# Kernel optimization log

Hardware: AMD Instinct MI355X
Metric: run time of the kernel (lower is better)

The kernel has to match this reference:

```python
import jax, jax.numpy as jnp
import numpy as np

NUM_BLOCKS = 32
B, S = 8, 2048


def setup_inputs() -> dict:
    key = jax.random.key(0)
    k1, k2, k3 = jax.random.split(key, 3)
    h = jax.random.uniform(k1, (B, S, NUM_BLOCKS, 4), dtype=jnp.float32)
    W = jax.random.uniform(k2, (B, S, NUM_BLOCKS, NUM_BLOCKS), dtype=jnp.float32)
    stim = jax.random.uniform(k3, (B, S, NUM_BLOCKS), dtype=jnp.float32)
    return {"h": h, "W": W, "stim": stim}


def _step(h, W, stim):
    nb = h.shape[-2]
    eye = jnp.eye(nb, dtype=W.dtype)
    W_no_self = W * (1.0 - eye)                      # zero self-connections
    # neighbor inflow: [b,s,i,j] @ [b,s,j,c] -> [b,s,i,c]
    inflow = jnp.einsum('bsij,bsjc->bsic', W_no_self, h)
    total_w = W_no_self.sum(axis=-1, keepdims=True) + 1e-8
    neigh = inflow / total_w                          # weighted neighbor mean

    E, P, G, L = h[..., 0], h[..., 1], h[..., 2], h[..., 3]
    En, Pn, Gn, Ln = neigh[..., 0], neigh[..., 1], neigh[..., 2], neigh[..., 3]

    clamp01 = lambda x: jnp.clip(x, 0.0, 1.0)
    E_new = clamp01(E + 0.3 * stim - 0.4 * P - 0.2 * G)
    P_new = clamp01(P + 0.5 * stim + 0.3 * (Pn - P) - 0.2 * E)
    G_new = clamp01(G + 0.4 * E * (1.0 - P) + 0.2 * (Gn - G) - 0.3 * P)
    good_neighbor = 0.5 * En + 0.5 * Gn
    L_new = clamp01(L + 0.4 * good_neighbor + 0.3 * (Ln - L) - 0.3 * P)

    h_new = jnp.stack([E_new, P_new, G_new, L_new], axis=-1)  # [b,s,nb,4]

    # pairwise euclidean distance over the 4 EPGL channels (torch.cdist p=2)
    diff = h_new[..., :, None, :] - h_new[..., None, :, :]    # [b,s,nb,nb,4]
    sq = jnp.sum(diff * diff, axis=-1)
    # safe sqrt: zero distance -> 0 (matches cdist; avoids nan grads)
    h_diff = jnp.where(sq > 0, jnp.sqrt(jnp.where(sq > 0, sq, 1.0)), 0.0)

    mutual_L = 0.5 * (L_new[..., :, None] + L_new[..., None, :])
    alpha, beta = 0.1 * mutual_L, 0.05
    W_new = W + alpha * h_diff - beta * W
    W_new = jnp.clip(W_new, 0.0, 1.0) * (1.0 - eye)
    return h_new, W_new


def reference(h, W, stim):
    return _step(h, W, stim)
```

## Files before the change

### kernel.cpp

```cpp
#include <hip/hip_runtime.h>

#define NB 32
#define WAVES_PER_BLOCK 4
#define TOKENS_PER_WAVE 4

__device__ __forceinline__ float clamp01(float x) {
    return fminf(fmaxf(x, 0.0f), 1.0f);
}

__device__ __forceinline__ void gload_lds16(const float* g, float* lds) {
    __builtin_amdgcn_global_load_lds(
        (const __attribute__((address_space(1))) void*)g,
        (__attribute__((address_space(3))) void*)lds, 16, 0, 0);
}
__device__ __forceinline__ void gload_lds4(const float* g, float* lds) {
    __builtin_amdgcn_global_load_lds(
        (const __attribute__((address_space(1))) void*)g,
        (__attribute__((address_space(3))) void*)lds, 4, 0, 0);
}

__device__ __forceinline__ void stage_token(
    const float* __restrict__ W, const float* __restrict__ h,
    int token, float* bufW, float* bufH, int lw)
{
    const float* Wt = W + (size_t)token * (NB * NB);
    #pragma unroll
    for (int k = 0; k < 4; ++k) {
        gload_lds16(Wt + (size_t)(k * 64 + lw) * 4, bufW + k * 256);
    }
    const float* ht = h + (size_t)token * (NB * 4);
    gload_lds4(ht + lw,      bufH);
    gload_lds4(ht + 64 + lw, bufH + 64);
}

__global__ __launch_bounds__(256, 4) void biotoken_step(
    const float* __restrict__ h,
    const float* __restrict__ W,
    const float* __restrict__ stim,
    float* __restrict__ out_h,
    float* __restrict__ out_W)
{
    const int lw   = threadIdx.x & 63;
    const int wave = threadIdx.x >> 6;
    const int tok0 = (blockIdx.x * WAVES_PER_BLOCK + wave) * TOKENS_PER_WAVE;
    const int i    = lw & 31;
    const int half = lw >> 5;

    __shared__ float s_W   [WAVES_PER_BLOCK][2][NB * NB];
    __shared__ float s_hin [WAVES_PER_BLOCK][2][NB * 4];
    __shared__ float s_hnew[WAVES_PER_BLOCK][NB * 4];

    stage_token(W, h, tok0, s_W[wave][0], s_hin[wave][0], lw);
    float stiC = stim[(size_t)tok0 * NB + i];
    float stiN = 0.0f;

    #pragma unroll
    for (int tt = 0; tt < TOKENS_PER_WAVE; ++tt) {
        const int cur   = tt & 1;
        const int token = tok0 + tt;

        __syncthreads();

        if (tt + 1 < TOKENS_PER_WAVE) {
            stage_token(W, h, token + 1, s_W[wave][cur ^ 1],
                        s_hin[wave][cur ^ 1], lw);
            stiN = stim[(size_t)(token + 1) * NB + i];
        }

        const float* bw   = s_W[wave][cur];
        const float* shin = s_hin[wave][cur];

        float accE = 0.f, accP = 0.f, accG = 0.f, accL = 0.f, tot = 0.f;
        #pragma unroll
        for (int t = 0; t < 16; ++t) {
            const int jj = (half << 4) | ((t + i) & 15);
            float w = bw[i * 32 + jj];
            w = (jj == i) ? 0.0f : w;
            const float4 hj = *(const float4*)&shin[jj * 4];
            accE = fmaf(w, hj.x, accE);
            accP = fmaf(w, hj.y, accP);
            accG = fmaf(w, hj.z, accG);
            accL = fmaf(w, hj.w, accL);
            tot += w;
        }
        accE += __shfl_xor(accE, 32);
        accP += __shfl_xor(accP, 32);
        accG += __shfl_xor(accG, 32);
        accL += __shfl_xor(accL, 32);
        tot  += __shfl_xor(tot,  32);

        const float inv = 1.0f / (tot + 1e-8f);
        const float En = accE * inv, Pn = accP * inv;
        const float Gn = accG * inv, Ln = accL * inv;

        const float4 hi = *(const float4*)&shin[i * 4];
        const float E = hi.x, P = hi.y, G = hi.z, L = hi.w;

        const float E_new = clamp01(E + 0.3f * stiC - 0.4f * P - 0.2f * G);
        const float P_new = clamp01(P + 0.5f * stiC + 0.3f * (Pn - P) - 0.2f * E);
        const float G_new = clamp01(G + 0.4f * E * (1.0f - P) + 0.2f * (Gn - G) - 0.3f * P);
        const float good  = 0.5f * En + 0.5f * Gn;
        const float L_new = clamp01(L + 0.4f * good + 0.3f * (Ln - L) - 0.3f * P);

        if (half == 0) {
            const float4 hn = make_float4(E_new, P_new, G_new, L_new);
            ((float4*)s_hnew[wave])[i] = hn;
            ((float4*)(out_h + (size_t)token * (NB * 4)))[i] = hn;
        }
        __builtin_amdgcn_wave_barrier();

        const float* shn = s_hnew[wave];
        float4* outWt = (float4*)(out_W + (size_t)token * (NB * NB));

        const int jb0 = (lw & 7) * 4;
        float4 hjv[4];
        #pragma unroll
        for (int e = 0; e < 4; ++e) {
            hjv[e] = *(const float4*)&shn[(jb0 + e) * 4];
        }

        #pragma unroll
        for (int k = 0; k < 4; ++k) {
            const int m = k * 64 + lw;
            const int r = m >> 3;
            const float4 wv = *(const float4*)&bw[(size_t)m * 4];
            const float4 hr = *(const float4*)&shn[r * 4];
            const float  Lr = hr.w;
            const float* wp = (const float*)&wv;
            float4 res;
            float* resp = &res.x;
            #pragma unroll
            for (int e = 0; e < 4; ++e) {
                const int j = jb0 + e;
                const float4 hj = hjv[e];
                const float dx = hr.x - hj.x;
                const float dy = hr.y - hj.y;
                const float dz = hr.z - hj.z;
                const float dw = hr.w - hj.w;
                const float sq = dx * dx + dy * dy + dz * dz + dw * dw;
                const float dist = sqrtf(sq);
                const float mutual = 0.5f * (Lr + hj.w);
                float wn = 0.95f * wp[e] + 0.1f * mutual * dist;
                wn = clamp01(wn);
                resp[e] = (j == r) ? 0.0f : wn;
            }
            outWt[m] = res;
        }

        stiC = stiN;
    }
}

extern "C" void kernel_launch(void* const* d_in, const int* in_sizes, int n_in,
                              void* d_out, int out_size, void* d_ws, size_t ws_size,
                              hipStream_t stream) {
    const float* h    = (const float*)d_in[0];
    const float* W    = (const float*)d_in[1];
    const float* stim = (const float*)d_in[2];

    const int tokens = in_sizes[2] / NB;
    float* out_h = (float*)d_out;
    float* out_W = (float*)d_out + (size_t)tokens * NB * 4;

    const int blocks = tokens / (WAVES_PER_BLOCK * TOKENS_PER_WAVE);
    biotoken_step<<<blocks, 256, 0, stream>>>(h, W, stim, out_h, out_W);
}
```

Baseline: 138.4 us.

## Single-buffer swizzled W staging, direct global W reread, raise occupancy

Drops the LDS double buffer in favour of one per-wave buffer. W is now staged with a rotated column layout so each lane can read contiguous float4 rows for the neighbour matvec, which is meant to reduce LDS bank conflicts. The weight-update phase reads W straight from global memory into registers instead of from LDS, and the next token's prefetch is issued after the h update. The smaller LDS footprint allows launch bounds of 6 blocks per CU. The cost is a second global read of W, which relies on L2 hits, and less overlap between the prefetch and the matvec.

```diff
diff --git a/kernel.cpp b/kernel.cpp
--- a/kernel.cpp
+++ b/kernel.cpp
@@ -19,21 +19,8 @@
         (__attribute__((address_space(3))) void*)lds, 4, 0, 0);
 }
 
-__device__ __forceinline__ void stage_token(
-    const float* __restrict__ W, const float* __restrict__ h,
-    int token, float* bufW, float* bufH, int lw)
-{
-    const float* Wt = W + (size_t)token * (NB * NB);
-    #pragma unroll
-    for (int k = 0; k < 4; ++k) {
-        gload_lds16(Wt + (size_t)(k * 64 + lw) * 4, bufW + k * 256);
-    }
-    const float* ht = h + (size_t)token * (NB * 4);
-    gload_lds4(ht + lw,      bufH);
-    gload_lds4(ht + 64 + lw, bufH + 64);
-}
 
-__global__ __launch_bounds__(256, 4) void biotoken_step(
+__global__ __launch_bounds__(256, 6) void biotoken_step(
     const float* __restrict__ h,
     const float* __restrict__ W,
     const float* __restrict__ stim,
@@ -46,42 +33,69 @@
     const int i    = lw & 31;
     const int half = lw >> 5;
 
-    __shared__ float s_W   [WAVES_PER_BLOCK][2][NB * NB];
-    __shared__ float s_hin [WAVES_PER_BLOCK][2][NB * 4];
+    __shared__ float s_W   [WAVES_PER_BLOCK][NB * NB];
+    __shared__ float s_hin [WAVES_PER_BLOCK][NB * 4];
     __shared__ float s_hnew[WAVES_PER_BLOCK][NB * 4];
 
-    stage_token(W, h, tok0, s_W[wave][0], s_hin[wave][0], lw);
+    float* bufW = s_W[wave];
+    float* bufH = s_hin[wave];
+    float* bufN = s_hnew[wave];
+
+    auto stage = [&](int token) {
+        const float* Wt = W + (size_t)token * (NB * NB);
+        #pragma unroll
+        for (int k = 0; k < 4; ++k) {
+            const int c  = k * 64 + lw;
+            const int j0 = c >> 5;
+            const int ii = ((c & 31) - 5 * j0) & 31;
+            gload_lds16(Wt + ii * NB + 4 * j0, bufW + k * 256);
+        }
+        const float* ht = h + (size_t)token * (NB * 4);
+        gload_lds4(ht + lw,      bufH);
+        gload_lds4(ht + 64 + lw, bufH + 64);
+    };
+
+    stage(tok0);
     float stiC = stim[(size_t)tok0 * NB + i];
     float stiN = 0.0f;
 
     #pragma unroll
     for (int tt = 0; tt < TOKENS_PER_WAVE; ++tt) {
-        const int cur   = tt & 1;
         const int token = tok0 + tt;
 
         __syncthreads();
 
-        if (tt + 1 < TOKENS_PER_WAVE) {
-            stage_token(W, h, token + 1, s_W[wave][cur ^ 1],
-                        s_hin[wave][cur ^ 1], lw);
-            stiN = stim[(size_t)(token + 1) * NB + i];
+        const float4* Wt4 = (const float4*)(W + (size_t)token * (NB * NB));
+        float4 wr[4];
+        wr[0] = Wt4[0 * 64 + lw];
+        wr[1] = Wt4[1 * 64 + lw];
+        wr[2] = Wt4[2 * 64 + lw];
+        wr[3] = Wt4[3 * 64 + lw];
+
+        float4 wv[4];
+        #pragma unroll
+        for (int q = 0; q < 4; ++q) {
+            const int j0v = half * 4 + q;
+            const int cc  = j0v * 32 + ((i + 5 * j0v) & 31);
+            wv[q] = *(const float4*)&bufW[4 * cc];
         }
-
-        const float* bw   = s_W[wave][cur];
-        const float* shin = s_hin[wave][cur];
 
         float accE = 0.f, accP = 0.f, accG = 0.f, accL = 0.f, tot = 0.f;
         #pragma unroll
-        for (int t = 0; t < 16; ++t) {
-            const int jj = (half << 4) | ((t + i) & 15);
-            float w = bw[i * 32 + jj];
-            w = (jj == i) ? 0.0f : w;
-            const float4 hj = *(const float4*)&shin[jj * 4];
-            accE = fmaf(w, hj.x, accE);
-            accP = fmaf(w, hj.y, accP);
-            accG = fmaf(w, hj.z, accG);
-            accL = fmaf(w, hj.w, accL);
-            tot += w;
+        for (int q = 0; q < 4; ++q) {
+            const float* wp = (const float*)&wv[q];
+            #pragma unroll
+            for (int dj = 0; dj < 4; ++dj) {
+                const int j = half * 16 + 4 * q + dj;
+                float w = wp[dj];
+                w = (j == i) ? 0.0f : w;
+                const float4 hj = *(const float4*)&bufH[j * 4];
+                accE = fmaf(w, hj.x, accE);
+                accP = fmaf(w, hj.y, accP);
+                accG = fmaf(w, hj.z, accG);
+                accL = fmaf(w, hj.w, accL);
+                tot += w;
+            }
         }
         accE += __shfl_xor(accE, 32);
         accP += __shfl_xor(accP, 32);
@@ -93,7 +107,7 @@
         const float En = accE * inv, Pn = accP * inv;
         const float Gn = accG * inv, Ln = accL * inv;
 
-        const float4 hi = *(const float4*)&shin[i * 4];
+        const float4 hi = *(const float4*)&bufH[i * 4];
         const float E = hi.x, P = hi.y, G = hi.z, L = hi.w;
 
         const float E_new = clamp01(E + 0.3f * stiC - 0.4f * P - 0.2f * G);
@@ -104,29 +118,32 @@
 
         if (half == 0) {
             const float4 hn = make_float4(E_new, P_new, G_new, L_new);
-            ((float4*)s_hnew[wave])[i] = hn;
+            ((float4*)bufN)[i] = hn;
             ((float4*)(out_h + (size_t)token * (NB * 4)))[i] = hn;
         }
-        __builtin_amdgcn_wave_barrier();
 
-        const float* shn = s_hnew[wave];
+        __builtin_amdgcn_sched_barrier(0);
+        if (tt + 1 < TOKENS_PER_WAVE) {
+            stage(token + 1);
+            stiN = stim[(size_t)(token + 1) * NB + i];
+        }
+        __builtin_amdgcn_sched_barrier(0);
+
         float4* outWt = (float4*)(out_W + (size_t)token * (NB * NB));
-
         const int jb0 = (lw & 7) * 4;
         float4 hjv[4];
         #pragma unroll
         for (int e = 0; e < 4; ++e) {
-            hjv[e] = *(const float4*)&shn[(jb0 + e) * 4];
+            hjv[e] = *(const float4*)&bufN[(jb0 + e) * 4];
         }
 
         #pragma unroll
         for (int k = 0; k < 4; ++k) {
             const int m = k * 64 + lw;
             const int r = m >> 3;
-            const float4 wv = *(const float4*)&bw[(size_t)m * 4];
-            const float4 hr = *(const float4*)&shn[r * 4];
+            const float4 hr = *(const float4*)&bufN[r * 4];
             const float  Lr = hr.w;
-            const float* wp = (const float*)&wv;
+            const float* wp = (const float*)&wr[k];
             float4 res;
             float* resp = &res.x;
             #pragma unroll
```

Result: slower. 168.3 us (+21.6%).
